# Kernel optimization log

Hardware: AMD Instinct MI355X
Metric: run time of the kernel (lower is better)

The kernel has to match this reference:

```python
import jax, jax.numpy as jnp
import numpy as np

HIDDEN = 2048
HEADS = 16
LN_EPS = 1e-5


def setup_inputs() -> dict:
    key = jax.random.key(0)
    ks = jax.random.split(key, 12)
    B, S, D = 4, 4096, HIDDEN
    std = 0.02
    inp = {
        "x": jax.random.normal(ks[0], (B, S, D), dtype=jnp.float32),
        "ln_g": jnp.ones((D,), dtype=jnp.float32),
        "ln_b": jnp.zeros((D,), dtype=jnp.float32),
        # weights stored as [in, out] so y = x @ W + b (equivalent to torch Linear)
        "Wq": jax.random.normal(ks[1], (D, D), dtype=jnp.float32) * std,
        "bq": jnp.zeros((D,), dtype=jnp.float32),
        "Wk": jax.random.normal(ks[2], (D, D), dtype=jnp.float32) * std,
        "bk": jnp.zeros((D,), dtype=jnp.float32),
        "Wv": jax.random.normal(ks[3], (D, D), dtype=jnp.float32) * std,
        "bv": jnp.zeros((D,), dtype=jnp.float32),
        "Wo": jax.random.normal(ks[4], (D, D), dtype=jnp.float32) * std,
        "bo": jnp.zeros((D,), dtype=jnp.float32),
    }
    return inp


def reference(x, ln_g, ln_b, Wq, bq, Wk, bk, Wv, bv, Wo, bo):
    B, S, D = x.shape
    H = HEADS
    hd = D // H
    # LayerNorm
    mu = jnp.mean(x, axis=-1, keepdims=True)
    var = jnp.mean(jnp.square(x - mu), axis=-1, keepdims=True)
    xn = (x - mu) * jax.lax.rsqrt(var + LN_EPS) * ln_g + ln_b
    # QKV projections
    q = (xn @ Wq + bq).reshape(B, S, H, hd)
    k = (xn @ Wk + bk).reshape(B, S, H, hd)
    v = (xn @ Wv + bv).reshape(B, S, H, hd)
    # Faithful to source: q @ k.transpose(-2,-1) on [B,S,H,hd] -> scores [B,S,H,H]
    # (attention mixes across heads per token; scale uses full hidden_dim)
    scores = jnp.einsum('bshd,bsgd->bshg', q, k) / jnp.sqrt(jnp.float32(D))
    weights = jax.nn.softmax(scores, axis=-1)
    context = jnp.einsum('bshg,bsgd->bshd', weights, v).reshape(B, S, D)
    out = context @ Wo + bo
    return out
```

## Files before the change

kernel.cpp:

```cpp
#include <hip/hip_runtime.h>

typedef __bf16 bf16x8 __attribute__((ext_vector_type(8)));
typedef __bf16 bf16x4 __attribute__((ext_vector_type(4)));
typedef float  f32x4  __attribute__((ext_vector_type(4)));

#define GLOAD_LDS16(g, l) \
  __builtin_amdgcn_global_load_lds((const __attribute__((address_space(1))) void*)(g), \
                                   (__attribute__((address_space(3))) void*)(l), 16, 0, 0)

__global__ __launch_bounds__(256) void wcvt_kernel(
    const float* __restrict__ W0, const float* __restrict__ W1,
    const float* __restrict__ W2, const float* __restrict__ W3,
    __bf16* __restrict__ WtBase)
{
  const float* W = (blockIdx.z == 0) ? W0 : (blockIdx.z == 1) ? W1 : (blockIdx.z == 2) ? W2 : W3;
  __bf16* dst = WtBase + (size_t)blockIdx.z * 2048 * 2048;
  __shared__ float tile[32][33];
  const int tx = threadIdx.x & 31, ty = threadIdx.x >> 5;
  const int gi = blockIdx.x * 32, gj = blockIdx.y * 32;
  #pragma unroll
  for (int r = 0; r < 32; r += 8)
    tile[ty + r][tx] = W[(size_t)(gi + ty + r) * 2048 + gj + tx];
  __syncthreads();
  #pragma unroll
  for (int r = 0; r < 32; r += 8)
    dst[(size_t)(gj + ty + r) * 2048 + gi + tx] = (__bf16)tile[tx][ty + r];
}

__global__ __launch_bounds__(256) void ln_kernel(
    const float* __restrict__ x, const float* __restrict__ gw,
    const float* __restrict__ bw, __bf16* __restrict__ xn)
{
  __shared__ float red[8];
  const size_t base = (size_t)blockIdx.x * 2048;
  const int t = threadIdx.x;
  float4 v0 = *(const float4*)(x + base + t * 4);
  float4 v1 = *(const float4*)(x + base + 1024 + t * 4);
  float sm = v0.x + v0.y + v0.z + v0.w + v1.x + v1.y + v1.z + v1.w;
  float sq = v0.x*v0.x + v0.y*v0.y + v0.z*v0.z + v0.w*v0.w
           + v1.x*v1.x + v1.y*v1.y + v1.z*v1.z + v1.w*v1.w;
  #pragma unroll
  for (int off = 32; off; off >>= 1) {
    sm += __shfl_down(sm, off);
    sq += __shfl_down(sq, off);
  }
  if ((t & 63) == 0) { red[t >> 6] = sm; red[4 + (t >> 6)] = sq; }
  __syncthreads();
  const float fs = red[0] + red[1] + red[2] + red[3];
  const float fq = red[4] + red[5] + red[6] + red[7];
  const float mu = fs * (1.f / 2048.f);
  const float var = fq * (1.f / 2048.f) - mu * mu;
  const float rs = rsqrtf(var + 1e-5f);
  float4 g0 = *(const float4*)(gw + t * 4);
  float4 g1 = *(const float4*)(gw + 1024 + t * 4);
  float4 b0 = *(const float4*)(bw + t * 4);
  float4 b1 = *(const float4*)(bw + 1024 + t * 4);
  bf16x4 o0, o1;
  o0[0] = (__bf16)((v0.x - mu) * rs * g0.x + b0.x);
  o0[1] = (__bf16)((v0.y - mu) * rs * g0.y + b0.y);
  o0[2] = (__bf16)((v0.z - mu) * rs * g0.z + b0.z);
  o0[3] = (__bf16)((v0.w - mu) * rs * g0.w + b0.w);
  o1[0] = (__bf16)((v1.x - mu) * rs * g1.x + b1.x);
  o1[1] = (__bf16)((v1.y - mu) * rs * g1.y + b1.y);
  o1[2] = (__bf16)((v1.z - mu) * rs * g1.z + b1.z);
  o1[3] = (__bf16)((v1.w - mu) * rs * g1.w + b1.w);
  *(bf16x4*)(xn + base + t * 4) = o0;
  *(bf16x4*)(xn + base + 1024 + t * 4) = o1;
}

template <int MODE>
__global__ __launch_bounds__(512, 2) void gemm256(
    const __bf16* __restrict__ A, int lda,
    const __bf16* __restrict__ WtBase,
    const float* __restrict__ b0, const float* __restrict__ b1,
    const float* __restrict__ b2, void* __restrict__ outp)
{
  __shared__ __attribute__((aligned(16))) char smem[131072];
  const int tid = threadIdx.x, lane = tid & 63, wid = tid >> 6;
  const int wm = wid >> 2, wn = wid & 3;
  const int m0 = blockIdx.x * 256;
  int which, n0;
  const __bf16* Bt;
  const float* bias;
  if (MODE == 0) {
    which = blockIdx.y >> 3;
    n0 = (blockIdx.y & 7) * 256;
    Bt = WtBase + (size_t)which * 2048 * 2048 + (size_t)n0 * 2048;
    bias = (which == 0) ? b0 : (which == 1) ? b1 : b2;
  } else {
    which = 0;
    n0 = blockIdx.y * 256;
    Bt = WtBase + (size_t)n0 * 2048;
    bias = b0;
  }

  const int srow = tid >> 3;
  const int segl = (tid & 7) ^ (srow & 7);
  const __bf16* Ag[4];
  const __bf16* Bg[4];
  #pragma unroll
  for (int g = 0; g < 4; g++) {
    Ag[g] = A  + (size_t)(m0 + g * 64 + srow) * lda  + segl * 8;
    Bg[g] = Bt + (size_t)(g * 64 + srow)      * 2048 + segl * 8;
  }
  const int ldst = __builtin_amdgcn_readfirstlane(wid * 1024);

#define STAGE_TILE(buf, kt)                                                  \
  do {                                                                       \
    const int koff_ = (kt) * 64;                                             \
    _Pragma("unroll") for (int g_ = 0; g_ < 4; g_++)                         \
      GLOAD_LDS16(Ag[g_] + koff_, smem + (buf) * 32768 + g_ * 8192 + ldst);  \
    _Pragma("unroll") for (int g_ = 0; g_ < 4; g_++)                         \
      GLOAD_LDS16(Bg[g_] + koff_, smem + 65536 + (buf) * 32768 + g_ * 8192 + ldst); \
  } while (0)

  const int fr = lane & 15, sl = lane >> 4, x78 = fr & 7;
  const int off0 = (sl ^ x78) * 16;
  const int off1 = ((4 + sl) ^ x78) * 16;
  const int abase = (wm * 128 + fr) * 128;
  const int bbase = (wn * 64 + fr) * 128;

  f32x4 acc[8][4];
  #pragma unroll
  for (int i = 0; i < 8; i++)
    #pragma unroll
    for (int j = 0; j < 4; j++) acc[i][j] = (f32x4){0.f, 0.f, 0.f, 0.f};

  STAGE_TILE(0, 0);
  const int NT = 2048 / 64;

  for (int t = 0; t < NT; t++) {
    const int c = t & 1;
    __builtin_amdgcn_s_barrier();
    if (t + 1 < NT) {
      STAGE_TILE(c ^ 1, t + 1);
      asm volatile("s_waitcnt vmcnt(8)" ::: "memory");
    } else {
      asm volatile("s_waitcnt vmcnt(0)" ::: "memory");
    }
    __builtin_amdgcn_s_barrier();
    const char* Ab = smem + c * 32768;
    const char* Bb = smem + 65536 + c * 32768;
    #pragma unroll
    for (int ks = 0; ks < 2; ks++) {
      const int ofk = ks ? off1 : off0;
      bf16x8 bfr[4];
      #pragma unroll
      for (int ni = 0; ni < 4; ni++)
        bfr[ni] = *(const bf16x8*)(Bb + bbase + ni * 2048 + ofk);
      #pragma unroll
      for (int mh = 0; mh < 2; mh++) {
        bf16x8 afr[4];
        #pragma unroll
        for (int i = 0; i < 4; i++)
          afr[i] = *(const bf16x8*)(Ab + abase + (mh * 4 + i) * 2048 + ofk);
        __builtin_amdgcn_s_setprio(1);
        #pragma unroll
        for (int i = 0; i < 4; i++)
          #pragma unroll
          for (int ni = 0; ni < 4; ni++)
            acc[mh * 4 + i][ni] =
                __builtin_amdgcn_mfma_f32_16x16x32_bf16(afr[i], bfr[ni], acc[mh * 4 + i][ni], 0, 0, 0);
        __builtin_amdgcn_s_setprio(0);
        if (!(ks == 1 && mh == 1)) __builtin_amdgcn_s_barrier();
      }
    }
  }
#undef STAGE_TILE

  const int colf = lane & 15, rowf = (lane >> 4) * 4;
  #pragma unroll
  for (int mi = 0; mi < 8; mi++) {
    const int rw = m0 + wm * 128 + mi * 16 + rowf;
    #pragma unroll
    for (int ni = 0; ni < 4; ni++) {
      const int cc = n0 + wn * 64 + ni * 16 + colf;
      const float bi = bias[cc];
      if (MODE == 0) {
        __bf16* qkv = (__bf16*)outp;
        #pragma unroll
        for (int j = 0; j < 4; j++)
          qkv[(size_t)(rw + j) * 6144 + (size_t)which * 2048 + cc] =
              (__bf16)(acc[mi][ni][j] + bi);
      } else {
        float* out = (float*)outp;
        #pragma unroll
        for (int j = 0; j < 4; j++)
          out[(size_t)(rw + j) * 2048 + cc] = acc[mi][ni][j] + bi;
      }
    }
  }
}

__global__ __launch_bounds__(256) void attn_kernel(__bf16* __restrict__ qkv)
{
  __shared__ __bf16 att[4 * 6144];
  __shared__ float Psh[4 * 256];
  const int tid = threadIdx.x, lane = tid & 63, w = tid >> 6;
  const size_t token = (size_t)blockIdx.x * 4 + w;
  const __bf16* src = qkv + token * 6144;
  char* ldsb = (char*)att;
  const int lbase = __builtin_amdgcn_readfirstlane(w * 12288);
  #pragma unroll
  for (int r = 0; r < 12; r++)
    GLOAD_LDS16(src + r * 512 + lane * 8, ldsb + lbase + r * 1024);
  __syncthreads();

  const __bf16* my = att + w * 6144;
  const int h = lane >> 2, gq = lane & 3;
  const __bf16* qrow = my + h * 128;
  float s[4] = {0.f, 0.f, 0.f, 0.f};
  for (int d = 0; d < 128; d += 8) {
    bf16x8 qv = *(const bf16x8*)(qrow + d);
    float qf[8];
    #pragma unroll
    for (int j = 0; j < 8; j++) qf[j] = (float)qv[j];
    #pragma unroll
    for (int i = 0; i < 4; i++) {
      bf16x8 kv = *(const bf16x8*)(my + 2048 + (gq * 4 + i) * 128 + d);
      #pragma unroll
      for (int j = 0; j < 8; j++) s[i] += qf[j] * (float)kv[j];
    }
  }
  const float scale = 0.022097086912079612f;
  #pragma unroll
  for (int i = 0; i < 4; i++) s[i] *= scale;
  float mx = fmaxf(fmaxf(s[0], s[1]), fmaxf(s[2], s[3]));
  mx = fmaxf(mx, __shfl_xor(mx, 1));
  mx = fmaxf(mx, __shfl_xor(mx, 2));
  float p[4], sum = 0.f;
  #pragma unroll
  for (int i = 0; i < 4; i++) { p[i] = __expf(s[i] - mx); sum += p[i]; }
  sum += __shfl_xor(sum, 1);
  sum += __shfl_xor(sum, 2);
  const float inv = 1.f / sum;
  #pragma unroll
  for (int i = 0; i < 4; i++) Psh[w * 256 + h * 16 + gq * 4 + i] = p[i] * inv;
  __syncthreads();

  const int h2 = lane >> 2, db = (lane & 3) * 32;
  const __bf16* vb = my + 4096;
  float acc[32];
  #pragma unroll
  for (int i = 0; i < 32; i++) acc[i] = 0.f;
  for (int g = 0; g < 16; g++) {
    const float pv = Psh[w * 256 + h2 * 16 + g];
    #pragma unroll
    for (int c = 0; c < 4; c++) {
      bf16x8 vv = *(const bf16x8*)(vb + g * 128 + db + c * 8);
      #pragma unroll
      for (int j = 0; j < 8; j++) acc[c * 8 + j] += pv * (float)vv[j];
    }
  }
  __bf16* dst = qkv + token * 6144 + h2 * 128 + db;
  #pragma unroll
  for (int c = 0; c < 4; c++) {
    bf16x8 ov;
    #pragma unroll
    for (int j = 0; j < 8; j++) ov[j] = (__bf16)acc[c * 8 + j];
    *(bf16x8*)(dst + c * 8) = ov;
  }
}

extern "C" void kernel_launch(void* const* d_in, const int* in_sizes, int n_in,
                              void* d_out, int out_size, void* d_ws, size_t ws_size,
                              hipStream_t stream)
{
  const float* x    = (const float*)d_in[0];
  const float* ln_g = (const float*)d_in[1];
  const float* ln_b = (const float*)d_in[2];
  const float* Wq   = (const float*)d_in[3];
  const float* bq   = (const float*)d_in[4];
  const float* Wk   = (const float*)d_in[5];
  const float* bk   = (const float*)d_in[6];
  const float* Wv   = (const float*)d_in[7];
  const float* bv   = (const float*)d_in[8];
  const float* Wo   = (const float*)d_in[9];
  const float* bo   = (const float*)d_in[10];
  float* out = (float*)d_out;
  const int M = in_sizes[0] / 2048;

  char* ws = (char*)d_ws;
  __bf16* Wt  = (__bf16*)ws;
  __bf16* qkv = (__bf16*)(ws + 33554432);
  __bf16* xn  = (__bf16*)d_out;

  wcvt_kernel<<<dim3(64, 64, 4), 256, 0, stream>>>(Wq, Wk, Wv, Wo, Wt);
  ln_kernel<<<M, 256, 0, stream>>>(x, ln_g, ln_b, xn);
  gemm256<0><<<dim3(M / 256, 24), 512, 0, stream>>>(xn, 2048, Wt, bq, bk, bv, (void*)qkv);
  attn_kernel<<<M / 4, 256, 0, stream>>>(qkv);
  gemm256<1><<<dim3(M / 256, 8), 512, 0, stream>>>(qkv, 6144, Wt + (size_t)3 * 2048 * 2048,
                                                   bo, nullptr, nullptr, (void*)out);
}
```

Measured before the change: 643.8 us.

## Switch GEMM mainloop to 4-stage K=32 pipeline with packed swizzled LDS layout

The GEMM main loop drops from K-tiles of 64 with double buffering to K-tiles of 32 with a four-buffer ring, three tiles in flight. Global-to-LDS loads use a new packed layout that puts two rows per 128-byte LDS line with an XOR swizzle, and the fragment address math is rewritten to match. The goal is to hide more global memory latency behind the MFMAs with deeper prefetch. The cost is twice as many loop iterations and barriers per K, and a more complex swizzle that could bring LDS bank conflicts.

```diff
diff --git a/kernel.cpp b/kernel.cpp
--- a/kernel.cpp
+++ b/kernel.cpp
@@ -94,31 +94,31 @@
     bias = b0;
   }
 
-  const int srow = tid >> 3;
-  const int segl = (tid & 7) ^ (srow & 7);
-  const __bf16* Ag[4];
-  const __bf16* Bg[4];
-  #pragma unroll
-  for (int g = 0; g < 4; g++) {
-    Ag[g] = A  + (size_t)(m0 + g * 64 + srow) * lda  + segl * 8;
-    Bg[g] = Bt + (size_t)(g * 64 + srow)      * 2048 + segl * 8;
-  }
+  const int ci0 = tid, ci1 = 512 + tid;
+  const int sr0 = ci0 >> 3, sg0 = (ci0 & 7) ^ (sr0 & 7);
+  const int sr1 = ci1 >> 3, sg1 = (ci1 & 7) ^ (sr1 & 7);
+  const int r0 = sr0 * 2 + (sg0 >> 2), c0 = (sg0 & 3) * 8;
+  const int r1 = sr1 * 2 + (sg1 >> 2), c1 = (sg1 & 3) * 8;
+  const __bf16* Ag0 = A + (size_t)(m0 + r0) * lda + c0;
+  const __bf16* Ag1 = A + (size_t)(m0 + r1) * lda + c1;
+  const __bf16* Bg0 = Bt + (size_t)r0 * 2048 + c0;
+  const __bf16* Bg1 = Bt + (size_t)r1 * 2048 + c1;
   const int ldst = __builtin_amdgcn_readfirstlane(wid * 1024);
 
-#define STAGE_TILE(buf, kt)                                                  \
-  do {                                                                       \
-    const int koff_ = (kt) * 64;                                             \
-    _Pragma("unroll") for (int g_ = 0; g_ < 4; g_++)                         \
-      GLOAD_LDS16(Ag[g_] + koff_, smem + (buf) * 32768 + g_ * 8192 + ldst);  \
-    _Pragma("unroll") for (int g_ = 0; g_ < 4; g_++)                         \
-      GLOAD_LDS16(Bg[g_] + koff_, smem + 65536 + (buf) * 32768 + g_ * 8192 + ldst); \
+#define STAGE(buf, kt)                                                        \
+  do {                                                                        \
+    const int ko_ = (kt) * 32;                                                \
+    GLOAD_LDS16(Ag0 + ko_, smem + (buf) * 32768 + ldst);                      \
+    GLOAD_LDS16(Ag1 + ko_, smem + (buf) * 32768 + 8192 + ldst);               \
+    GLOAD_LDS16(Bg0 + ko_, smem + (buf) * 32768 + 16384 + ldst);              \
+    GLOAD_LDS16(Bg1 + ko_, smem + (buf) * 32768 + 16384 + 8192 + ldst);       \
   } while (0)
 
-  const int fr = lane & 15, sl = lane >> 4, x78 = fr & 7;
-  const int off0 = (sl ^ x78) * 16;
-  const int off1 = ((4 + sl) ^ x78) * 16;
-  const int abase = (wm * 128 + fr) * 128;
-  const int bbase = (wn * 64 + fr) * 128;
+  const int fr = lane & 15, sl = lane >> 4;
+  const int slogf = sl | ((fr & 1) << 2);
+  const int rbA = wm * 128 + fr, rbB = wn * 64 + fr;
+  const int abase = (rbA >> 1) * 128 + ((slogf ^ ((rbA >> 1) & 7)) * 16);
+  const int bbase = (rbB >> 1) * 128 + ((slogf ^ ((rbB >> 1) & 7)) * 16);
 
   f32x4 acc[8][4];
   #pragma unroll
@@ -126,47 +126,50 @@
     #pragma unroll
     for (int j = 0; j < 4; j++) acc[i][j] = (f32x4){0.f, 0.f, 0.f, 0.f};
 
-  STAGE_TILE(0, 0);
-  const int NT = 2048 / 64;
+  STAGE(0, 0);
+  STAGE(1, 1);
+  STAGE(2, 2);
+  const int NT = 2048 / 32;
 
   for (int t = 0; t < NT; t++) {
-    const int c = t & 1;
+    const int br = t & 3;
     __builtin_amdgcn_s_barrier();
-    if (t + 1 < NT) {
-      STAGE_TILE(c ^ 1, t + 1);
-      asm volatile("s_waitcnt vmcnt(8)" ::: "memory");
+    if (t + 3 < NT) {
+      STAGE((t + 3) & 3, t + 3);
+      asm volatile("s_waitcnt vmcnt(12)" ::: "memory");
     } else {
       asm volatile("s_waitcnt vmcnt(0)" ::: "memory");
     }
     __builtin_amdgcn_s_barrier();
-    const char* Ab = smem + c * 32768;
-    const char* Bb = smem + 65536 + c * 32768;
-    #pragma unroll
-    for (int ks = 0; ks < 2; ks++) {
-      const int ofk = ks ? off1 : off0;
-      bf16x8 bfr[4];
+    const char* Ab = smem + br * 32768;
+    const char* Bb = Ab + 16384;
+    bf16x8 bfr[4], afr[4];
+    #pragma unroll
+    for (int ni = 0; ni < 4; ni++)
+      bfr[ni] = *(const bf16x8*)(Bb + bbase + ni * 1024);
+    #pragma unroll
+    for (int i = 0; i < 4; i++)
+      afr[i] = *(const bf16x8*)(Ab + abase + i * 1024);
+    __builtin_amdgcn_s_setprio(1);
+    #pragma unroll
+    for (int i = 0; i < 4; i++)
       #pragma unroll
       for (int ni = 0; ni < 4; ni++)
-        bfr[ni] = *(const bf16x8*)(Bb + bbase + ni * 2048 + ofk);
-      #pragma unroll
-      for (int mh = 0; mh < 2; mh++) {
-        bf16x8 afr[4];
-        #pragma unroll
-        for (int i = 0; i < 4; i++)
-          afr[i] = *(const bf16x8*)(Ab + abase + (mh * 4 + i) * 2048 + ofk);
-        __builtin_amdgcn_s_setprio(1);
-        #pragma unroll
-        for (int i = 0; i < 4; i++)
-          #pragma unroll
-          for (int ni = 0; ni < 4; ni++)
-            acc[mh * 4 + i][ni] =
-                __builtin_amdgcn_mfma_f32_16x16x32_bf16(afr[i], bfr[ni], acc[mh * 4 + i][ni], 0, 0, 0);
-        __builtin_amdgcn_s_setprio(0);
-        if (!(ks == 1 && mh == 1)) __builtin_amdgcn_s_barrier();
-      }
-    }
-  }
-#undef STAGE_TILE
+        acc[i][ni] = __builtin_amdgcn_mfma_f32_16x16x32_bf16(afr[i], bfr[ni], acc[i][ni], 0, 0, 0);
+    __builtin_amdgcn_s_setprio(0);
+    __builtin_amdgcn_s_barrier();
+    #pragma unroll
+    for (int i = 0; i < 4; i++)
+      afr[i] = *(const bf16x8*)(Ab + abase + 4096 + i * 1024);
+    __builtin_amdgcn_s_setprio(1);
+    #pragma unroll
+    for (int i = 0; i < 4; i++)
+      #pragma unroll
+      for (int ni = 0; ni < 4; ni++)
+        acc[4 + i][ni] = __builtin_amdgcn_mfma_f32_16x16x32_bf16(afr[i], bfr[ni], acc[4 + i][ni], 0, 0, 0);
+    __builtin_amdgcn_s_setprio(0);
+  }
+#undef STAGE
 
   const int colf = lane & 15, rowf = (lane >> 4) * 4;
   #pragma unroll
```

After: 696.8 us. 8.2% more time.
